# Kernel optimization log

Measured on AMD Instinct MI355X. Metric: run time of the kernel, lower is better.

The kernel has to match this reference:

```python
import jax, jax.numpy as jnp
import numpy as np

N_TOKENS = 8192
TOP_K = 2
N_EXPERTS = 8
D_MODEL = 1024
D_FF = 2048
CAPACITY = 3072  # static per-expert buffer; mean load 2048, overflow prob ~0
FP8_MAX = 448.0


def setup_inputs() -> dict:
    key = jax.random.key(0)
    ks = jax.random.split(key, 6)
    x = jax.random.normal(ks[0], (N_TOKENS, D_MODEL), dtype=jnp.float32)
    expert_indices = jax.random.randint(ks[1], (N_TOKENS, TOP_K), 0, N_EXPERTS)
    expert_weights = jax.nn.softmax(jax.random.normal(ks[2], (N_TOKENS, TOP_K)), axis=-1).astype(jnp.float32)
    # trunc_normal init, std = sqrt(1/3)/sqrt(fan_in), fan_in = w.shape[1]
    std_in = (1.0 / 3.0) ** 0.5 / D_MODEL ** 0.5
    std_ff = (1.0 / 3.0) ** 0.5 / D_FF ** 0.5
    w1 = jnp.clip(jax.random.normal(ks[3], (N_EXPERTS, D_MODEL, D_FF), jnp.float32) * std_in, -2 * std_in, 2 * std_in)
    w2 = jnp.clip(jax.random.normal(ks[4], (N_EXPERTS, D_MODEL, D_FF), jnp.float32) * std_in, -2 * std_in, 2 * std_in)
    w3 = jnp.clip(jax.random.normal(ks[5], (N_EXPERTS, D_FF, D_MODEL), jnp.float32) * std_ff, -2 * std_ff, 2 * std_ff)
    return {"x": x, "expert_indices": expert_indices, "expert_weights": expert_weights,
            "w1": w1, "w2": w2, "w3": w3}


def reference(x, expert_indices, expert_weights, w1, w2, w3):
    n_tokens, d_model = x.shape
    top_k = expert_indices.shape[1]
    n_experts = w1.shape[0]

    # input fp8 scale (buffer fill_ in torch -> no grad)
    input_scale = jax.lax.stop_gradient(FP8_MAX / (jnp.max(jnp.abs(x)) + 1e-12) * 0.9)
    # w*_scale buffers are ones at inference (recalibration happens only randomly in training)
    w_scale = jnp.float32(1.0)

    # ---- dispatch: stable sort assignments by expert, compute slot positions ----
    flat_experts = expert_indices.reshape(-1)                       # [N*K]
    flat_weights = expert_weights.reshape(-1)                       # [N*K]
    token_indices = jnp.repeat(jnp.arange(n_tokens), top_k)         # [N*K]
    order = jnp.argsort(flat_experts)                               # stable sort
    sorted_experts = flat_experts[order]
    sorted_weights = flat_weights[order]
    sorted_tokens = token_indices[order]
    counts = jnp.bincount(flat_experts, length=n_experts)           # [E]
    seg_starts = jnp.cumsum(counts) - counts                        # [E]
    positions = jnp.arange(n_tokens * top_k) - seg_starts[sorted_experts]

    # scatter tokens into padded per-expert buffers [E, CAP, d]; OOB slots dropped
    padded = jnp.zeros((n_experts, CAPACITY, d_model), x.dtype)
    padded = padded.at[sorted_experts, positions].set(x[sorted_tokens], mode='drop')

    # ---- grouped SwiGLU with fp8-style quant/dequant scaling ----
    inp_scaled = jnp.clip(padded * input_scale, -FP8_MAX, FP8_MAX)  # [E, C, d]
    w1_s = jnp.clip(w1 * w_scale, -FP8_MAX, FP8_MAX)
    w2_s = jnp.clip(w2 * w_scale, -FP8_MAX, FP8_MAX)
    w3_s = jnp.clip(w3 * w_scale, -FP8_MAX, FP8_MAX)
    gate = jnp.einsum('ecd,edf->ecf', inp_scaled, w1_s) / (input_scale * w_scale)
    gate = jax.nn.silu(gate)
    value = jnp.einsum('ecd,edf->ecf', inp_scaled, w2_s) / (input_scale * w_scale)
    hidden = gate * value                                            # [E, C, f]
    # per-expert hidden amax (padded rows are zero -> same max as valid rows)
    hidden_amax = jnp.max(jnp.abs(hidden), axis=(1, 2))              # [E]
    hidden_scale = (FP8_MAX / (hidden_amax + 1e-12) * 0.9)[:, None, None]
    hidden_scaled = jnp.clip(hidden * hidden_scale, -FP8_MAX, FP8_MAX)
    out_padded = jnp.einsum('ecf,efd->ecd', hidden_scaled, w3_s) / (hidden_scale * w_scale)

    # ---- combine: gather per-assignment outputs, weight, scatter-add per token ----
    valid = positions < CAPACITY
    gathered = out_padded[sorted_experts, jnp.minimum(positions, CAPACITY - 1)]
    gathered = gathered * jnp.where(valid, sorted_weights, 0.0)[:, None]
    output = jnp.zeros((n_tokens, d_model), x.dtype).at[sorted_tokens].add(gathered)
    return output
```

## Files before the change

kernel.cpp:

```cpp
#include <hip/hip_runtime.h>

#define N_TOK   8192
#define TOPK    2
#define N_EXP   8
#define DM      1024
#define DFF     2048
#define CAP     3072

typedef __attribute__((ext_vector_type(8))) short bf16x8;
typedef __attribute__((ext_vector_type(4))) float f32x4;

__device__ __forceinline__ unsigned short f2bf(float x) {
    union { float f; unsigned u; } un; un.f = x;
    unsigned r = un.u + 0x7fffu + ((un.u >> 16) & 1u);
    return (unsigned short)(r >> 16);
}

__device__ __forceinline__ void glds16(const void* g, void* l) {
    __builtin_amdgcn_global_load_lds(
        (const __attribute__((address_space(1))) unsigned int*)g,
        (__attribute__((address_space(3))) unsigned int*)l, 16, 0, 0);
}

__global__ void cvt_x_kernel(const float4* __restrict__ x, ushort4* __restrict__ xb) {
    int i = blockIdx.x * 256 + threadIdx.x;
    float4 v = x[i];
    ushort4 o;
    o.x = f2bf(v.x); o.y = f2bf(v.y); o.z = f2bf(v.z); o.w = f2bf(v.w);
    xb[i] = o;
}

__global__ void transpose_cvt64_kernel(const float* __restrict__ inA, const float* __restrict__ inB,
                                       unsigned short* __restrict__ outA, unsigned short* __restrict__ outB,
                                       int R, int C) {
    __shared__ unsigned short L[64][72];
    const int z = blockIdx.z;
    const float* in = (z & 8) ? inB : inA;
    unsigned short* out = (z & 8) ? outB : outA;
    const int e = z & 7;
    const int r0 = blockIdx.y * 64, c0 = blockIdx.x * 64;
    const int t = threadIdx.x;
    const int rr = t >> 4;
    const int cv = t & 15;
    const float4* src = (const float4*)(in + ((size_t)e * R + r0) * C + c0);
    const int c4 = C >> 2;
#pragma unroll
    for (int i = 0; i < 4; i++) {
        int r = rr + 16 * i;
        float4 v = src[(size_t)r * c4 + cv];
        L[r][cv * 4 + 0] = f2bf(v.x);
        L[r][cv * 4 + 1] = f2bf(v.y);
        L[r][cv * 4 + 2] = f2bf(v.z);
        L[r][cv * 4 + 3] = f2bf(v.w);
    }
    __syncthreads();
    unsigned short* dst = out + ((size_t)e * C + c0) * R + r0;
    const int cc = t >> 4;
    const int rv = t & 15;
#pragma unroll
    for (int i = 0; i < 4; i++) {
        int c = cc + 16 * i;
        ushort4 o;
        o.x = L[rv * 4 + 0][c];
        o.y = L[rv * 4 + 1][c];
        o.z = L[rv * 4 + 2][c];
        o.w = L[rv * 4 + 3][c];
        *(ushort4*)(dst + (size_t)c * R + rv * 4) = o;
    }
}

__global__ void dispatch_kernel(const int* __restrict__ eidx, const float* __restrict__ ewt,
                                int* __restrict__ counts, int* __restrict__ row_token,
                                float* __restrict__ row_weight) {
    int i = blockIdx.x * 256 + threadIdx.x;
    if (i < N_TOK * TOPK) {
        int e = eidx[i];
        int pos = atomicAdd(&counts[e], 1);
        if (pos < CAP) {
            row_token[e * CAP + pos] = i >> 1;
            row_weight[e * CAP + pos] = ewt[i];
        }
    }
}

__global__ __launch_bounds__(256, 2)
void gemm1_kernel(const unsigned short* __restrict__ xb, const unsigned short* __restrict__ w1t,
                  const unsigned short* __restrict__ w2t, const int* __restrict__ counts,
                  const int* __restrict__ row_token, unsigned short* __restrict__ hidden) {
    const int e = blockIdx.z;
    const int r0 = blockIdx.y * 128;
    if (r0 >= counts[e]) return;
    const int f0 = blockIdx.x * 128;

    __shared__ unsigned short lA[128 * 32];
    __shared__ unsigned short lB1[128 * 32];
    __shared__ unsigned short lB2[128 * 32];

    const int t = threadIdx.x;
    const int lane = t & 63;
    const int wave = t >> 6;

    const int rstage = t >> 2;
    const int cs = (t & 3) ^ ((rstage >> 1) & 3);
    const int kbyte = cs * 16;

    const int tok0 = row_token[e * CAP + r0 + rstage];
    const int tok1 = row_token[e * CAP + r0 + 64 + rstage];
    const char* pA0 = (const char*)(xb + (size_t)tok0 * DM) + kbyte;
    const char* pA1 = (const char*)(xb + (size_t)tok1 * DM) + kbyte;
    const char* pB1a = (const char*)(w1t + ((size_t)e * DFF + f0 + rstage) * DM) + kbyte;
    const char* pB1b = pB1a + (size_t)64 * DM * 2;
    const char* pB2a = (const char*)(w2t + ((size_t)e * DFF + f0 + rstage) * DM) + kbyte;
    const char* pB2b = pB2a + (size_t)64 * DM * 2;

    char* lAp = (char*)lA + t * 16;
    char* lB1p = (char*)lB1 + t * 16;
    char* lB2p = (char*)lB2 + t * 16;

    const int mw = (wave & 1) * 64;
    const int nw = (wave >> 1) * 64;
    const int l15 = lane & 15;
    const int lq = lane >> 4;
    const int swz = (l15 >> 1) & 3;
    const unsigned short* aBase  = lA  + (mw + l15) * 32 + ((lq ^ swz) * 8);
    const unsigned short* b1Base = lB1 + (nw + l15) * 32 + ((lq ^ swz) * 8);
    const unsigned short* b2Base = lB2 + (nw + l15) * 32 + ((lq ^ swz) * 8);

    f32x4 accG[4][4];
    f32x4 accV[4][4];
#pragma unroll
    for (int i = 0; i < 4; i++)
#pragma unroll
        for (int j = 0; j < 4; j++) {
            accG[i][j] = (f32x4){0.f, 0.f, 0.f, 0.f};
            accV[i][j] = (f32x4){0.f, 0.f, 0.f, 0.f};
        }

    for (int k0 = 0; k0 < DM; k0 += 32) {
        glds16(pA0, lAp);            glds16(pA1, lAp + 4096);
        glds16(pB1a, lB1p);          glds16(pB1b, lB1p + 4096);
        glds16(pB2a, lB2p);          glds16(pB2b, lB2p + 4096);
        pA0 += 64; pA1 += 64; pB1a += 64; pB1b += 64; pB2a += 64; pB2b += 64;
        __syncthreads();

        bf16x8 a[4], b1[4], b2[4];
#pragma unroll
        for (int i = 0; i < 4; i++) {
            a[i]  = *(const bf16x8*)(aBase  + i * 512);
            b1[i] = *(const bf16x8*)(b1Base + i * 512);
            b2[i] = *(const bf16x8*)(b2Base + i * 512);
        }
#pragma unroll
        for (int i = 0; i < 4; i++)
#pragma unroll
            for (int j = 0; j < 4; j++) {
                accG[i][j] = __builtin_amdgcn_mfma_f32_16x16x32_bf16(a[i], b1[j], accG[i][j], 0, 0, 0);
                accV[i][j] = __builtin_amdgcn_mfma_f32_16x16x32_bf16(a[i], b2[j], accV[i][j], 0, 0, 0);
            }
        __syncthreads();
    }

    const size_t hbase = ((size_t)e * CAP + r0) * DFF + f0;
#pragma unroll
    for (int i = 0; i < 4; i++)
#pragma unroll
        for (int j = 0; j < 4; j++)
#pragma unroll
            for (int r = 0; r < 4; r++) {
                int m = mw + i * 16 + lq * 4 + r;
                int n = nw + j * 16 + l15;
                float g = accG[i][j][r];
                float v = accV[i][j][r];
                float h = (g / (1.f + __expf(-g))) * v;
                hidden[hbase + (size_t)m * DFF + n] = f2bf(h);
            }
}

__global__ __launch_bounds__(256, 2)
void gemm2_kernel(const unsigned short* __restrict__ hidden, const unsigned short* __restrict__ w3t,
                  const int* __restrict__ counts, const int* __restrict__ row_token,
                  const float* __restrict__ row_weight, float* __restrict__ out) {
    const int e = blockIdx.z;
    const int r0 = blockIdx.y * 128;
    if (r0 >= counts[e]) return;
    const int d0 = blockIdx.x * 128;

    __shared__ unsigned short lA[128 * 32];
    __shared__ unsigned short lB[128 * 32];

    const int t = threadIdx.x;
    const int lane = t & 63;
    const int wave = t >> 6;

    const int rstage = t >> 2;
    const int cs = (t & 3) ^ ((rstage >> 1) & 3);
    const int kbyte = cs * 16;

    const char* pA0 = (const char*)(hidden + ((size_t)e * CAP + r0 + rstage) * DFF) + kbyte;
    const char* pA1 = pA0 + (size_t)64 * DFF * 2;
    const char* pB0 = (const char*)(w3t + ((size_t)e * DM + d0 + rstage) * DFF) + kbyte;
    const char* pB1 = pB0 + (size_t)64 * DFF * 2;

    char* lAp = (char*)lA + t * 16;
    char* lBp = (char*)lB + t * 16;

    const int mw = (wave & 1) * 64;
    const int nw = (wave >> 1) * 64;
    const int l15 = lane & 15;
    const int lq = lane >> 4;
    const int swz = (l15 >> 1) & 3;
    const unsigned short* aBase = lA + (mw + l15) * 32 + ((lq ^ swz) * 8);
    const unsigned short* bBase = lB + (nw + l15) * 32 + ((lq ^ swz) * 8);

    f32x4 acc[4][4];
#pragma unroll
    for (int i = 0; i < 4; i++)
#pragma unroll
        for (int j = 0; j < 4; j++) acc[i][j] = (f32x4){0.f, 0.f, 0.f, 0.f};

    for (int k0 = 0; k0 < DFF; k0 += 32) {
        glds16(pA0, lAp);  glds16(pA1, lAp + 4096);
        glds16(pB0, lBp);  glds16(pB1, lBp + 4096);
        pA0 += 64; pA1 += 64; pB0 += 64; pB1 += 64;
        __syncthreads();

        bf16x8 a[4], b[4];
#pragma unroll
        for (int i = 0; i < 4; i++) {
            a[i] = *(const bf16x8*)(aBase + i * 512);
            b[i] = *(const bf16x8*)(bBase + i * 512);
        }
#pragma unroll
        for (int i = 0; i < 4; i++)
#pragma unroll
            for (int j = 0; j < 4; j++)
                acc[i][j] = __builtin_amdgcn_mfma_f32_16x16x32_bf16(a[i], b[j], acc[i][j], 0, 0, 0);
        __syncthreads();
    }

    const float* rw = row_weight + e * CAP + r0;
    const int* rt = row_token + e * CAP + r0;
#pragma unroll
    for (int i = 0; i < 4; i++)
#pragma unroll
        for (int r = 0; r < 4; r++) {
            int m = mw + i * 16 + lq * 4 + r;
            float w = rw[m];
            if (w != 0.f) {
                int tok = rt[m];
                float* orow = out + (size_t)tok * DM + d0 + nw + l15;
#pragma unroll
                for (int j = 0; j < 4; j++)
                    atomicAdd(orow + j * 16, acc[i][j][r] * w);
            }
        }
}

extern "C" void kernel_launch(void* const* d_in, const int* in_sizes, int n_in,
                              void* d_out, int out_size, void* d_ws, size_t ws_size,
                              hipStream_t stream) {
    const float* x = (const float*)d_in[0];
    const int* eidx = (const int*)d_in[1];
    const float* ewt = (const float*)d_in[2];
    const float* w1 = (const float*)d_in[3];
    const float* w2 = (const float*)d_in[4];
    const float* w3 = (const float*)d_in[5];
    float* out = (float*)d_out;

    char* ws = (char*)d_ws;
    size_t off = 0;
    auto alloc = [&](size_t b) { size_t o = off; off += (b + 255) & ~(size_t)255; return o; };
    int*   counts     = (int*)(ws + alloc(N_EXP * 4));
    int*   row_token  = (int*)(ws + alloc((size_t)N_EXP * CAP * 4));
    float* row_weight = (float*)(ws + alloc((size_t)N_EXP * CAP * 4));
    size_t hdr_end = off;
    unsigned short* xb  = (unsigned short*)(ws + alloc((size_t)N_TOK * DM * 2));
    unsigned short* w1t = (unsigned short*)(ws + alloc((size_t)N_EXP * DFF * DM * 2));
    unsigned short* w2t = (unsigned short*)(ws + alloc((size_t)N_EXP * DFF * DM * 2));
    unsigned short* w3t = (unsigned short*)(ws + alloc((size_t)N_EXP * DM * DFF * 2));
    unsigned short* hidden = (unsigned short*)(ws + alloc((size_t)N_EXP * CAP * DFF * 2));
    (void)ws_size; (void)in_sizes; (void)n_in;

    hipMemsetAsync(d_out, 0, (size_t)out_size * sizeof(float), stream);
    hipMemsetAsync(ws, 0, hdr_end, stream);

    cvt_x_kernel<<<(N_TOK * DM / 4) / 256, 256, 0, stream>>>((const float4*)x, (ushort4*)xb);
    transpose_cvt64_kernel<<<dim3(DFF / 64, DM / 64, 16), 256, 0, stream>>>(w1, w2, w1t, w2t, DM, DFF);
    transpose_cvt64_kernel<<<dim3(DM / 64, DFF / 64, 8), 256, 0, stream>>>(w3, w3, w3t, w3t, DFF, DM);
    dispatch_kernel<<<(N_TOK * TOPK) / 256, 256, 0, stream>>>(eidx, ewt, counts, row_token, row_weight);

    gemm1_kernel<<<dim3(DFF / 128, CAP / 128, N_EXP), 256, 0, stream>>>(xb, w1t, w2t, counts, row_token, hidden);
    gemm2_kernel<<<dim3(DM / 128, CAP / 128, N_EXP), 256, 0, stream>>>(hidden, w3t, counts, row_token, row_weight, out);
}
```

Before: 641.8 us.

## Narrow gemm1 N-tile and replace atomic scatter with per-slot rows plus combine

Gemm1 now uses a 128x64 output tile (half the B tiles, fewer accumulators), and both GEMMs raise launch bounds to 3 blocks per SM for higher occupancy. Gemm2 no longer does fp32 atomicAdd into the output. It writes weighted bf16 rows per slot into a buffer that reuses the w1t workspace, and a new combine kernel gathers each token's two slots. This removes atomic contention and the output memset, at the cost of an extra kernel, an extra round trip through bf16 rows with some precision loss, and more A-tile reloads in gemm1.

```diff
diff --git a/kernel.cpp b/kernel.cpp
--- a/kernel.cpp
+++ b/kernel.cpp
@@ -14,6 +14,9 @@
     union { float f; unsigned u; } un; un.f = x;
     unsigned r = un.u + 0x7fffu + ((un.u >> 16) & 1u);
     return (unsigned short)(r >> 16);
+}
+__device__ __forceinline__ float bf2f(unsigned short u) {
+    union { unsigned u; float f; } c; c.u = ((unsigned)u) << 16; return c.f;
 }
 
 __device__ __forceinline__ void glds16(const void* g, void* l) {
@@ -71,30 +74,33 @@
 
 __global__ void dispatch_kernel(const int* __restrict__ eidx, const float* __restrict__ ewt,
                                 int* __restrict__ counts, int* __restrict__ row_token,
-                                float* __restrict__ row_weight) {
+                                float* __restrict__ row_weight, int* __restrict__ slot_of) {
     int i = blockIdx.x * 256 + threadIdx.x;
     if (i < N_TOK * TOPK) {
         int e = eidx[i];
         int pos = atomicAdd(&counts[e], 1);
+        int slot = -1;
         if (pos < CAP) {
-            row_token[e * CAP + pos] = i >> 1;
-            row_weight[e * CAP + pos] = ewt[i];
-        }
-    }
-}
-
-__global__ __launch_bounds__(256, 2)
+            slot = e * CAP + pos;
+            row_token[slot] = i >> 1;
+            row_weight[slot] = ewt[i];
+        }
+        slot_of[i] = slot;
+    }
+}
+
+__global__ __launch_bounds__(256, 3)
 void gemm1_kernel(const unsigned short* __restrict__ xb, const unsigned short* __restrict__ w1t,
                   const unsigned short* __restrict__ w2t, const int* __restrict__ counts,
                   const int* __restrict__ row_token, unsigned short* __restrict__ hidden) {
     const int e = blockIdx.z;
     const int r0 = blockIdx.y * 128;
     if (r0 >= counts[e]) return;
-    const int f0 = blockIdx.x * 128;
+    const int f0 = blockIdx.x * 64;
 
     __shared__ unsigned short lA[128 * 32];
-    __shared__ unsigned short lB1[128 * 32];
-    __shared__ unsigned short lB2[128 * 32];
+    __shared__ unsigned short lB1[64 * 32];
+    __shared__ unsigned short lB2[64 * 32];
 
     const int t = threadIdx.x;
     const int lane = t & 63;
@@ -108,17 +114,15 @@
     const int tok1 = row_token[e * CAP + r0 + 64 + rstage];
     const char* pA0 = (const char*)(xb + (size_t)tok0 * DM) + kbyte;
     const char* pA1 = (const char*)(xb + (size_t)tok1 * DM) + kbyte;
-    const char* pB1a = (const char*)(w1t + ((size_t)e * DFF + f0 + rstage) * DM) + kbyte;
-    const char* pB1b = pB1a + (size_t)64 * DM * 2;
-    const char* pB2a = (const char*)(w2t + ((size_t)e * DFF + f0 + rstage) * DM) + kbyte;
-    const char* pB2b = pB2a + (size_t)64 * DM * 2;
+    const char* pB1 = (const char*)(w1t + ((size_t)e * DFF + f0 + rstage) * DM) + kbyte;
+    const char* pB2 = (const char*)(w2t + ((size_t)e * DFF + f0 + rstage) * DM) + kbyte;
 
     char* lAp = (char*)lA + t * 16;
     char* lB1p = (char*)lB1 + t * 16;
     char* lB2p = (char*)lB2 + t * 16;
 
     const int mw = (wave & 1) * 64;
-    const int nw = (wave >> 1) * 64;
+    const int nw = (wave >> 1) * 32;
     const int l15 = lane & 15;
     const int lq = lane >> 4;
     const int swz = (l15 >> 1) & 3;
@@ -126,34 +130,35 @@
     const unsigned short* b1Base = lB1 + (nw + l15) * 32 + ((lq ^ swz) * 8);
     const unsigned short* b2Base = lB2 + (nw + l15) * 32 + ((lq ^ swz) * 8);
 
-    f32x4 accG[4][4];
-    f32x4 accV[4][4];
+    f32x4 accG[4][2];
+    f32x4 accV[4][2];
 #pragma unroll
     for (int i = 0; i < 4; i++)
 #pragma unroll
-        for (int j = 0; j < 4; j++) {
+        for (int j = 0; j < 2; j++) {
             accG[i][j] = (f32x4){0.f, 0.f, 0.f, 0.f};
             accV[i][j] = (f32x4){0.f, 0.f, 0.f, 0.f};
         }
 
     for (int k0 = 0; k0 < DM; k0 += 32) {
-        glds16(pA0, lAp);            glds16(pA1, lAp + 4096);
-        glds16(pB1a, lB1p);          glds16(pB1b, lB1p + 4096);
-        glds16(pB2a, lB2p);          glds16(pB2b, lB2p + 4096);
-        pA0 += 64; pA1 += 64; pB1a += 64; pB1b += 64; pB2a += 64; pB2b += 64;
+        glds16(pA0, lAp);  glds16(pA1, lAp + 4096);
+        glds16(pB1, lB1p);
+        glds16(pB2, lB2p);
+        pA0 += 64; pA1 += 64; pB1 += 64; pB2 += 64;
         __syncthreads();
 
-        bf16x8 a[4], b1[4], b2[4];
-#pragma unroll
-        for (int i = 0; i < 4; i++) {
-            a[i]  = *(const bf16x8*)(aBase  + i * 512);
-            b1[i] = *(const bf16x8*)(b1Base + i * 512);
-            b2[i] = *(const bf16x8*)(b2Base + i * 512);
+        bf16x8 a[4], b1[2], b2[2];
+#pragma unroll
+        for (int i = 0; i < 4; i++) a[i] = *(const bf16x8*)(aBase + i * 512);
+#pragma unroll
+        for (int j = 0; j < 2; j++) {
+            b1[j] = *(const bf16x8*)(b1Base + j * 512);
+            b2[j] = *(const bf16x8*)(b2Base + j * 512);
         }
 #pragma unroll
         for (int i = 0; i < 4; i++)
 #pragma unroll
-            for (int j = 0; j < 4; j++) {
+            for (int j = 0; j < 2; j++) {
                 accG[i][j] = __builtin_amdgcn_mfma_f32_16x16x32_bf16(a[i], b1[j], accG[i][j], 0, 0, 0);
                 accV[i][j] = __builtin_amdgcn_mfma_f32_16x16x32_bf16(a[i], b2[j], accV[i][j], 0, 0, 0);
             }
@@ -164,7 +169,7 @@
 #pragma unroll
     for (int i = 0; i < 4; i++)
 #pragma unroll
-        for (int j = 0; j < 4; j++)
+        for (int j = 0; j < 2; j++)
 #pragma unroll
             for (int r = 0; r < 4; r++) {
                 int m = mw + i * 16 + lq * 4 + r;
@@ -176,10 +181,10 @@
             }
 }
 
-__global__ __launch_bounds__(256, 2)
+__global__ __launch_bounds__(256, 3)
 void gemm2_kernel(const unsigned short* __restrict__ hidden, const unsigned short* __restrict__ w3t,
-                  const int* __restrict__ counts, const int* __restrict__ row_token,
-                  const float* __restrict__ row_weight, float* __restrict__ out) {
+                  const int* __restrict__ counts, const float* __restrict__ row_weight,
+                  unsigned short* __restrict__ out_rows) {
     const int e = blockIdx.z;
     const int r0 = blockIdx.y * 128;
     if (r0 >= counts[e]) return;
@@ -239,21 +244,36 @@
     }
 
     const float* rw = row_weight + e * CAP + r0;
-    const int* rt = row_token + e * CAP + r0;
 #pragma unroll
     for (int i = 0; i < 4; i++)
 #pragma unroll
         for (int r = 0; r < 4; r++) {
             int m = mw + i * 16 + lq * 4 + r;
             float w = rw[m];
-            if (w != 0.f) {
-                int tok = rt[m];
-                float* orow = out + (size_t)tok * DM + d0 + nw + l15;
-#pragma unroll
-                for (int j = 0; j < 4; j++)
-                    atomicAdd(orow + j * 16, acc[i][j][r] * w);
-            }
-        }
+            unsigned short* orow = out_rows + ((size_t)(e * CAP + r0 + m)) * DM + d0 + nw + l15;
+#pragma unroll
+            for (int j = 0; j < 4; j++)
+                orow[j * 16] = f2bf(acc[i][j][r] * w);
+        }
+}
+
+__global__ void combine_kernel(const int* __restrict__ slot_of,
+                               const unsigned short* __restrict__ out_rows,
+                               float4* __restrict__ out) {
+    const int tok = blockIdx.x;
+    const int t = threadIdx.x;
+    const int s0 = slot_of[2 * tok];
+    const int s1 = slot_of[2 * tok + 1];
+    float4 acc = {0.f, 0.f, 0.f, 0.f};
+    if (s0 >= 0) {
+        ushort4 r = ((const ushort4*)(out_rows + (size_t)s0 * DM))[t];
+        acc.x += bf2f(r.x); acc.y += bf2f(r.y); acc.z += bf2f(r.z); acc.w += bf2f(r.w);
+    }
+    if (s1 >= 0) {
+        ushort4 r = ((const ushort4*)(out_rows + (size_t)s1 * DM))[t];
+        acc.x += bf2f(r.x); acc.y += bf2f(r.y); acc.z += bf2f(r.z); acc.w += bf2f(r.w);
+    }
+    out[(size_t)tok * (DM / 4) + t] = acc;
 }
 
 extern "C" void kernel_launch(void* const* d_in, const int* in_sizes, int n_in,
@@ -274,21 +294,23 @@
     int*   row_token  = (int*)(ws + alloc((size_t)N_EXP * CAP * 4));
     float* row_weight = (float*)(ws + alloc((size_t)N_EXP * CAP * 4));
     size_t hdr_end = off;
+    int*   slot_of    = (int*)(ws + alloc((size_t)N_TOK * TOPK * 4));
     unsigned short* xb  = (unsigned short*)(ws + alloc((size_t)N_TOK * DM * 2));
     unsigned short* w1t = (unsigned short*)(ws + alloc((size_t)N_EXP * DFF * DM * 2));
     unsigned short* w2t = (unsigned short*)(ws + alloc((size_t)N_EXP * DFF * DM * 2));
     unsigned short* w3t = (unsigned short*)(ws + alloc((size_t)N_EXP * DM * DFF * 2));
     unsigned short* hidden = (unsigned short*)(ws + alloc((size_t)N_EXP * CAP * DFF * 2));
+    unsigned short* out_rows = w1t;
     (void)ws_size; (void)in_sizes; (void)n_in;
 
-    hipMemsetAsync(d_out, 0, (size_t)out_size * sizeof(float), stream);
     hipMemsetAsync(ws, 0, hdr_end, stream);
 
     cvt_x_kernel<<<(N_TOK * DM / 4) / 256, 256, 0, stream>>>((const float4*)x, (ushort4*)xb);
     transpose_cvt64_kernel<<<dim3(DFF / 64, DM / 64, 16), 256, 0, stream>>>(w1, w2, w1t, w2t, DM, DFF);
     transpose_cvt64_kernel<<<dim3(DM / 64, DFF / 64, 8), 256, 0, stream>>>(w3, w3, w3t, w3t, DFF, DM);
-    dispatch_kernel<<<(N_TOK * TOPK) / 256, 256, 0, stream>>>(eidx, ewt, counts, row_token, row_weight);
-
-    gemm1_kernel<<<dim3(DFF / 128, CAP / 128, N_EXP), 256, 0, stream>>>(xb, w1t, w2t, counts, row_token, hidden);
-    gemm2_kernel<<<dim3(DM / 128, CAP / 128, N_EXP), 256, 0, stream>>>(hidden, w3t, counts, row_token, row_weight, out);
-}
+    dispatch_kernel<<<(N_TOK * TOPK) / 256, 256, 0, stream>>>(eidx, ewt, counts, row_token, row_weight, slot_of);
+
+    gemm1_kernel<<<dim3(DFF / 64, CAP / 128, N_EXP), 256, 0, stream>>>(xb, w1t, w2t, counts, row_token, hidden);
+    gemm2_kernel<<<dim3(DM / 128, CAP / 128, N_EXP), 256, 0, stream>>>(hidden, w3t, counts, row_weight, out_rows);
+    combine_kernel<<<N_TOK, 256, 0, stream>>>(slot_of, out_rows, (float4*)out);
+}
```

After: 594.6 us. -7.4%, faster.
